# Kernel tuning notes

Measured on AMD Instinct MI355X. Metric: run time of the kernel, lower is better.

Reference implementation:

```python
import jax, jax.numpy as jnp
import numpy as np

ROPE_BASE = 1000.0  # note: module uses base=1000, not the usual 10000


def _rope(x):
    # x: [B, L, H, d]; rotates the full head dim (x_pass is empty since d == hid_head)
    d = x.shape[-1]
    L = x.shape[1]
    theta = 1.0 / (ROPE_BASE ** (jnp.arange(0, d, 2, dtype=jnp.float32) / d))  # [d/2]
    idx = jnp.arange(L, dtype=jnp.float32)[:, None] * theta[None, :]            # [L, d/2]
    idx2 = jnp.concatenate([idx, idx], axis=-1)                                 # [L, d]
    cos = jnp.cos(idx2)[:, None, :]  # [L, 1, d] -> broadcasts over B, H
    sin = jnp.sin(idx2)[:, None, :]
    half = d // 2
    neg_half = jnp.concatenate([-x[..., half:], x[..., :half]], axis=-1)
    return x * cos + neg_half * sin


def setup_inputs() -> dict:
    key = jax.random.key(0)
    ks = jax.random.split(key, 8)
    B, Lq, Lc, F = 4, 1024, 2047, 2048
    s = 0.02
    return {
        "kv": jax.random.normal(ks[0], (B, 1, F), jnp.float32),
        "q": jax.random.normal(ks[1], (B, Lq, F), jnp.float32),
        "kv_cache": jax.random.normal(ks[2], (B, Lc, F, 2), jnp.float32),
        "Wq": jax.random.normal(ks[3], (F, F), jnp.float32) * s,
        "Wk": jax.random.normal(ks[4], (F, F), jnp.float32) * s,
        "Wv": jax.random.normal(ks[5], (F, F), jnp.float32) * s,
        "Wo": jax.random.normal(ks[6], (F, F), jnp.float32) * s,
        "mask": jnp.ones((B, 1, Lq, Lc + 1), jnp.int32),
        "num_heads": 16,
    }


def reference(kv, q, kv_cache, Wq, Wk, Wv, Wo, mask, num_heads):
    B = q.shape[0]
    F = Wq.shape[1]
    hd = F // num_heads

    query = q @ Wq                          # [B, Lq, F]
    key_new = kv[:, -1, :] @ Wk             # [B, F] (only last kv token is projected)
    val_new = kv[:, -1, :] @ Wv             # [B, F]

    key = jnp.concatenate([kv_cache[..., 0], key_new[:, None, :]], axis=1)    # [B, Lk, F]
    value = jnp.concatenate([kv_cache[..., 1], val_new[:, None, :]], axis=1)  # [B, Lk, F]
    kv_cache_out = jnp.stack([key, value], axis=-1)                            # [B, Lk, F, 2]

    query = query.reshape(B, -1, num_heads, hd)   # [B, Lq, H, d]
    key = key.reshape(B, -1, num_heads, hd)       # [B, Lk, H, d]
    value = value.reshape(B, -1, num_heads, hd)   # [B, Lk, H, d]

    query = _rope(query)
    key = _rope(key)

    aw = jnp.einsum('bqhd,bkhd->bhqk', query, key) / jnp.sqrt(jnp.float32(hd))
    aw = jnp.where(mask > 0, aw, -jnp.inf)  # mask [B,1,Lq,Lk] broadcasts over heads
    aw = jax.nn.softmax(aw, axis=-1)

    out = jnp.einsum('bhqk,bkhd->bqhd', aw, value).reshape(B, -1, F)
    logits = out @ Wo
    return logits, kv_cache_out
```

## Files before the change

### kernel.cpp

```cpp
#include <hip/hip_runtime.h>

#define B_  4
#define LQ  1024
#define LC  2047
#define LK  2048
#define F_  2048
#define H_  16
#define DH  128
#define NT  (LK / 64)

typedef __attribute__((ext_vector_type(4))) float f32x4;
typedef __attribute__((ext_vector_type(8))) __bf16 bf16x8;
typedef __attribute__((ext_vector_type(8))) unsigned short u16x8;

#define GLD16(gp, lp)                                                          \
  __builtin_amdgcn_global_load_lds(                                            \
      (const __attribute__((address_space(1))) void*)(gp),                     \
      (__attribute__((address_space(3))) void*)(lp), 16, 0, 0)

__device__ __forceinline__ unsigned short f2bf(float f) {
  unsigned u = __float_as_uint(f);
  u += 0x7FFFu + ((u >> 16) & 1u);
  return (unsigned short)(u >> 16);
}
__device__ __forceinline__ float bf2f(unsigned short u) {
  return __uint_as_float((unsigned)u << 16);
}
__device__ __forceinline__ unsigned pack_bf2(float a, float b) {
  return (__float_as_uint(b) & 0xffff0000u) | (__float_as_uint(a) >> 16);
}

__global__ void k_tables(float* __restrict__ cost, float* __restrict__ sint) {
  int idx = blockIdx.x * 256 + threadIdx.x;
  int pos = idx >> 6, j = idx & 63;
  float theta = powf(1000.0f, -(float)j / 64.0f);
  float a = (float)pos * theta;
  cost[idx] = cosf(a);
  sint[idx] = sinf(a);
}

__global__ void k_gemv_part(const float* __restrict__ kv, const float* __restrict__ Wk,
                            const float* __restrict__ Wv, float* __restrict__ part) {
  __shared__ float kvs[4][256];
  int tid = threadIdx.x, z = blockIdx.z;
#pragma unroll
  for (int b = 0; b < 4; ++b) kvs[b][tid] = kv[b * F_ + z * 256 + tid];
  __syncthreads();
  const float* W = blockIdx.y ? Wv : Wk;
  int col = blockIdx.x * 256 + tid;
  float a0 = 0.f, a1 = 0.f, a2 = 0.f, a3 = 0.f;
  for (int k = 0; k < 256; ++k) {
    float w = W[(size_t)(z * 256 + k) * F_ + col];
    a0 = fmaf(kvs[0][k], w, a0);
    a1 = fmaf(kvs[1][k], w, a1);
    a2 = fmaf(kvs[2][k], w, a2);
    a3 = fmaf(kvs[3][k], w, a3);
  }
  float* o = part + (size_t)(blockIdx.y * 8 + z) * 8192;
  o[col] = a0; o[2048 + col] = a1; o[4096 + col] = a2; o[6144 + col] = a3;
}

__global__ void k_prep_kv(const float* __restrict__ cache, const float* __restrict__ gpart,
                          const float* __restrict__ cost, const float* __restrict__ sint,
                          float* __restrict__ cache_out,
                          unsigned short* __restrict__ Kr, unsigned short* __restrict__ Vb) {
  int t = blockIdx.x * 256 + threadIdx.x;
  int j = t & 63, h = (t >> 6) & 15, pos = (t >> 10) & 2047, b = t >> 21;
  int f = h * DH + j;
  float k1, v1, k2, v2;
  if (pos < LC) {
    const float* p = cache + ((size_t)(b * LC + pos) * F_ + f) * 2;
    float2 x = *(const float2*)p;
    float2 y = *(const float2*)(p + 128);
    k1 = x.x; v1 = x.y; k2 = y.x; v2 = y.y;
  } else {
    float s0 = 0.f, s1 = 0.f, s2 = 0.f, s3 = 0.f;
#pragma unroll
    for (int z = 0; z < 8; ++z) {
      const float* gk = gpart + (size_t)z * 8192 + b * 2048;
      const float* gv = gpart + (size_t)(8 + z) * 8192 + b * 2048;
      s0 += gk[f]; s1 += gk[f + 64];
      s2 += gv[f]; s3 += gv[f + 64];
    }
    k1 = s0; k2 = s1; v1 = s2; v2 = s3;
  }
  float* o = cache_out + ((size_t)(b * LK + pos) * F_ + f) * 2;
  *(float2*)o = make_float2(k1, v1);
  *(float2*)(o + 128) = make_float2(k2, v2);
  float c = cost[pos * 64 + j], s = sint[pos * 64 + j];
  size_t kb = ((size_t)(b * H_ + h) * LK + pos) * DH + j;
  Kr[kb]      = f2bf(k1 * c - k2 * s);
  Kr[kb + 64] = f2bf(k2 * c + k1 * s);
  Vb[kb]      = f2bf(v1);
  Vb[kb + 64] = f2bf(v2);
}

__global__ void k_transpose_w(const float* __restrict__ Wq, const float* __restrict__ Wo,
                              unsigned short* __restrict__ WqT, unsigned short* __restrict__ WoT) {
  __shared__ float tile[32][33];
  const float* W = blockIdx.z ? Wo : Wq;
  unsigned short* Wt = blockIdx.z ? WoT : WqT;
  int n0 = blockIdx.x * 32, k0 = blockIdx.y * 32;
  int tx = threadIdx.x & 31, ty = threadIdx.x >> 5;
#pragma unroll
  for (int p = 0; p < 4; ++p)
    tile[ty + p * 8][tx] = W[(size_t)(k0 + ty + p * 8) * F_ + n0 + tx];
  __syncthreads();
#pragma unroll
  for (int p = 0; p < 4; ++p)
    Wt[(size_t)(n0 + ty + p * 8) * F_ + k0 + tx] = f2bf(tile[tx][ty + p * 8]);
}

__global__ void k_q_bf16(const float* __restrict__ x, unsigned short* __restrict__ y) {
  int t = blockIdx.x * 256 + threadIdx.x;
  float4 v = ((const float4*)x)[t];
  ushort4 o;
  o.x = f2bf(v.x); o.y = f2bf(v.y); o.z = f2bf(v.z); o.w = f2bf(v.w);
  ((ushort4*)y)[t] = o;
}

template <int MODE>
__launch_bounds__(256)
__global__ void k_gemm(const unsigned short* __restrict__ A, const unsigned short* __restrict__ Bt,
                       void* __restrict__ Cv, const float* __restrict__ cost,
                       const float* __restrict__ sint, int M, int N, int K) {
  __shared__ __align__(16) unsigned short SMEM[16640];
  unsigned short* As = SMEM;
  unsigned short* Bs = SMEM + 4096;
  int tid = threadIdx.x, wid = tid >> 6, l = tid & 63;
  int wm = wid >> 1, wn = wid & 1;
  int lr = l & 15, lg = l >> 4;
  int m0 = blockIdx.y * 128, n0 = blockIdx.x * 128;
  int row0 = tid >> 2, ch = tid & 3;
  const unsigned short* ga0 = A  + (size_t)(m0 + row0) * K + ch * 8;
  const unsigned short* ga1 = A  + (size_t)(m0 + row0 + 64) * K + ch * 8;
  const unsigned short* gb0 = Bt + (size_t)(n0 + row0) * K + ch * 8;
  const unsigned short* gb1 = Bt + (size_t)(n0 + row0 + 64) * K + ch * 8;
  f32x4 acc[4][4];
#pragma unroll
  for (int i = 0; i < 4; ++i)
#pragma unroll
    for (int j = 0; j < 4; ++j) acc[i][j] = (f32x4){0.f, 0.f, 0.f, 0.f};

  for (int kt = 0; kt < K; kt += 32) {
    __syncthreads();
    GLD16(ga0 + kt, As + tid * 8);
    GLD16(ga1 + kt, As + (tid + 256) * 8);
    GLD16(gb0 + kt, Bs + tid * 8);
    GLD16(gb1 + kt, Bs + (tid + 256) * 8);
    __syncthreads();
    bf16x8 af[4], bfr[4];
#pragma unroll
    for (int i = 0; i < 4; ++i) {
      af[i]  = *(const bf16x8*)&As[(wm * 64 + i * 16 + lr) * 32 + lg * 8];
      bfr[i] = *(const bf16x8*)&Bs[(wn * 64 + i * 16 + lr) * 32 + lg * 8];
    }
    __builtin_amdgcn_s_setprio(1);
#pragma unroll
    for (int mi = 0; mi < 4; ++mi)
#pragma unroll
      for (int ni = 0; ni < 4; ++ni)
        acc[mi][ni] = __builtin_amdgcn_mfma_f32_16x16x32_bf16(af[mi], bfr[ni], acc[mi][ni], 0, 0, 0);
    __builtin_amdgcn_s_setprio(0);
  }

  if (MODE == 0) {
#pragma unroll
    for (int mi = 0; mi < 4; ++mi)
#pragma unroll
      for (int ni = 0; ni < 4; ++ni) {
        int row = m0 + wm * 64 + mi * 16 + lg * 4;
        int col = n0 + wn * 64 + ni * 16 + lr;
#pragma unroll
        for (int r = 0; r < 4; ++r)
          ((float*)Cv)[(size_t)(row + r) * N + col] = acc[mi][ni][r];
      }
  } else {
    unsigned short* X = SMEM;
    __syncthreads();
#pragma unroll
    for (int mi = 0; mi < 4; ++mi)
#pragma unroll
      for (int ni = 0; ni < 4; ++ni) {
        int lrow = wm * 64 + mi * 16 + lg * 4;
        int col = wn * 64 + ni * 16 + lr;
#pragma unroll
        for (int r = 0; r < 4; ++r)
          X[(lrow + r) * 130 + col] = f2bf(acc[mi][ni][r]);
      }
    __syncthreads();
    int h = blockIdx.x;
    const float scale = 0.12751743343788055f;
    unsigned short* Q = (unsigned short*)Cv;
#pragma unroll
    for (int mi = 0; mi < 4; ++mi) {
      int lrow0 = wm * 64 + mi * 16 + lg * 4;
#pragma unroll
      for (int r = 0; r < 4; ++r) {
        int lrow = lrow0 + r;
        int grow = m0 + lrow;
        int qi = grow & 1023, b = grow >> 10;
        size_t obase = ((size_t)(b * H_ + h) * LQ + qi) * DH;
#pragma unroll
        for (int ni = 0; ni < 4; ++ni) {
          int col = wn * 64 + ni * 16 + lr;
          int jj = col & 63;
          float c = cost[qi * 64 + jj], s = sint[qi * 64 + jj];
          float a = acc[mi][ni][r];
          float a2 = bf2f(X[lrow * 130 + (col ^ 64)]);
          float o = (col < 64) ? (a * c - a2 * s) : (a * c + a2 * s);
          Q[obase + col] = f2bf(o * scale);
        }
      }
    }
  }
}

__launch_bounds__(256, 2)
__global__ void k_attn(const unsigned short* __restrict__ Qr, const unsigned short* __restrict__ Kr,
                       const unsigned short* __restrict__ Vb, unsigned short* __restrict__ Oo) {
  __shared__ __align__(16) unsigned short KsB[2][64 * 128];
  __shared__ __align__(16) unsigned short Vt[128][72];
  __shared__ __align__(16) unsigned short Pb[4][32][72];
  int tid = threadIdx.x, wid = tid >> 6, l = tid & 63;
  int lr = l & 15, lg = l >> 4;
  int bh = blockIdx.x, q0 = blockIdx.y * 128 + wid * 32;
  const unsigned short* Qb = Qr + ((size_t)bh * LQ + q0) * DH;
  const unsigned short* Kb = Kr + (size_t)bh * LK * DH;
  const unsigned short* Vp = Vb + (size_t)bh * LK * DH;

  bf16x8 qf[2][4];
#pragma unroll
  for (int s = 0; s < 2; ++s)
#pragma unroll
    for (int c = 0; c < 4; ++c)
      qf[s][c] = *(const bf16x8*)(Qb + (size_t)(s * 16 + lr) * DH + c * 32 + lg * 8);

  int gkoff[4], lkoff[4];
#pragma unroll
  for (int p = 0; p < 4; ++p) {
    int g = tid + p * 256, row = g >> 4, cc = g & 15;
    gkoff[p] = row * DH + (cc ^ (row & 15)) * 8;
    lkoff[p] = g * 8;
  }

  f32x4 oacc[2][8];
#pragma unroll
  for (int s = 0; s < 2; ++s)
#pragma unroll
    for (int i = 0; i < 8; ++i) oacc[s][i] = (f32x4){0.f, 0.f, 0.f, 0.f};
  float mrun[2][4] = {{-1e30f, -1e30f, -1e30f, -1e30f}, {-1e30f, -1e30f, -1e30f, -1e30f}};
  float lpart[2][4] = {{0.f, 0.f, 0.f, 0.f}, {0.f, 0.f, 0.f, 0.f}};

  int kp = tid >> 4, cg = tid & 15;

#pragma unroll
  for (int p = 0; p < 4; ++p) GLD16(Kb + gkoff[p], &KsB[0][lkoff[p]]);
  const unsigned short* vs0 = Vp + (size_t)kp * DH + cg * 8;
  u16x8 v00 = *(const u16x8*)(vs0);
  u16x8 v01 = *(const u16x8*)(vs0 + 16 * DH);
  u16x8 v10 = *(const u16x8*)(vs0 + 32 * DH);
  u16x8 v11 = *(const u16x8*)(vs0 + 48 * DH);

  for (int kt = 0; kt < NT; ++kt) {
    int cur = kt & 1;
    asm volatile("s_waitcnt vmcnt(0)" ::: "memory");
    __builtin_amdgcn_sched_barrier(0);
    __builtin_amdgcn_s_barrier();
    __builtin_amdgcn_sched_barrier(0);

#pragma unroll
    for (int pp = 0; pp < 2; ++pp) {
      int j = kp + pp * 16;
      int kks = j ^ ((cg & 7) << 2);
      u16x8 a = pp ? v10 : v00, b2 = pp ? v11 : v01;
#pragma unroll
      for (int e = 0; e < 8; ++e) {
        unsigned pack = (unsigned)a[e] | ((unsigned)b2[e] << 16);
        *(unsigned*)&Vt[cg * 8 + e][kks * 2] = pack;
      }
    }
    {
      const unsigned short* Kn = Kb + (size_t)((kt + 1 < NT) ? (kt + 1) * 64 * DH : 0);
#pragma unroll
      for (int p = 0; p < 4; ++p) GLD16(Kn + gkoff[p], &KsB[cur ^ 1][lkoff[p]]);
    }
    {
      int tn = (kt + 1 < NT) ? kt + 1 : kt;
      const unsigned short* vn = Vp + (size_t)(tn * 64 + kp) * DH + cg * 8;
      v00 = *(const u16x8*)(vn);
      v01 = *(const u16x8*)(vn + 16 * DH);
      v10 = *(const u16x8*)(vn + 32 * DH);
      v11 = *(const u16x8*)(vn + 48 * DH);
    }
    asm volatile("s_waitcnt lgkmcnt(0)" ::: "memory");
    __builtin_amdgcn_sched_barrier(0);
    __builtin_amdgcn_s_barrier();
    __builtin_amdgcn_sched_barrier(0);

    const unsigned short* Kcur = KsB[cur];
    f32x4 sf[2][4];
    __builtin_amdgcn_s_setprio(1);
#pragma unroll
    for (int ct = 0; ct < 4; ++ct) {
      f32x4 s0 = (f32x4){0.f, 0.f, 0.f, 0.f};
      f32x4 s1 = (f32x4){0.f, 0.f, 0.f, 0.f};
#pragma unroll
      for (int ck = 0; ck < 4; ++ck) {
        bf16x8 kf = *(const bf16x8*)&Kcur[(ct * 16 + lr) * 128 + (((ck * 4 + lg) ^ lr) << 3)];
        s0 = __builtin_amdgcn_mfma_f32_16x16x32_bf16(qf[0][ck], kf, s0, 0, 0, 0);
        s1 = __builtin_amdgcn_mfma_f32_16x16x32_bf16(qf[1][ck], kf, s1, 0, 0, 0);
      }
      sf[0][ct] = s0; sf[1][ct] = s1;
    }
    __builtin_amdgcn_s_setprio(0);

    float pmax[2][4];
    bool allok = true;
#pragma unroll
    for (int s = 0; s < 2; ++s)
#pragma unroll
      for (int r = 0; r < 4; ++r) {
        pmax[s][r] = fmaxf(fmaxf(sf[s][0][r], sf[s][1][r]), fmaxf(sf[s][2][r], sf[s][3][r]));
        allok = allok && (pmax[s][r] - mrun[s][r] <= 8.0f);
      }
    if (!__all(allok)) {
#pragma unroll
      for (int s = 0; s < 2; ++s)
#pragma unroll
        for (int r = 0; r < 4; ++r) {
          float m = pmax[s][r];
#pragma unroll
          for (int off = 1; off < 16; off <<= 1) m = fmaxf(m, __shfl_xor(m, off));
          float mnew = fmaxf(mrun[s][r], m);
          float scl = exp2f(mrun[s][r] - mnew);
          lpart[s][r] *= scl;
#pragma unroll
          for (int dt = 0; dt < 8; ++dt) oacc[s][dt][r] *= scl;
          mrun[s][r] = mnew;
        }
    }
#pragma unroll
    for (int s = 0; s < 2; ++s)
#pragma unroll
      for (int r = 0; r < 4; ++r) {
        float p0 = exp2f(sf[s][0][r] - mrun[s][r]);
        float p1 = exp2f(sf[s][1][r] - mrun[s][r]);
        float p2 = exp2f(sf[s][2][r] - mrun[s][r]);
        float p3 = exp2f(sf[s][3][r] - mrun[s][r]);
        lpart[s][r] += (p0 + p1) + (p2 + p3);
        unsigned* row = (unsigned*)&Pb[wid][s * 16 + lg * 4 + r][0];
        row[lr]      = pack_bf2(p0, p1);
        row[16 + lr] = pack_bf2(p2, p3);
      }

    bf16x8 pf00 = *(const bf16x8*)&Pb[wid][lr][lg * 8];
    bf16x8 pf01 = *(const bf16x8*)&Pb[wid][lr][32 + lg * 8];
    bf16x8 pf10 = *(const bf16x8*)&Pb[wid][16 + lr][lg * 8];
    bf16x8 pf11 = *(const bf16x8*)&Pb[wid][16 + lr][32 + lg * 8];
    __builtin_amdgcn_s_setprio(1);
#pragma unroll
    for (int dt = 0; dt < 8; ++dt) {
      int d = dt * 16 + lr;
      int x = (d >> 3) & 7;
      bf16x8 v0 = *(const bf16x8*)&Vt[d][(lg ^ x) << 3];
      bf16x8 v1 = *(const bf16x8*)&Vt[d][((4 + lg) ^ x) << 3];
      oacc[0][dt] = __builtin_amdgcn_mfma_f32_16x16x32_bf16(pf00, v0, oacc[0][dt], 0, 0, 0);
      oacc[0][dt] = __builtin_amdgcn_mfma_f32_16x16x32_bf16(pf01, v1, oacc[0][dt], 0, 0, 0);
      oacc[1][dt] = __builtin_amdgcn_mfma_f32_16x16x32_bf16(pf10, v0, oacc[1][dt], 0, 0, 0);
      oacc[1][dt] = __builtin_amdgcn_mfma_f32_16x16x32_bf16(pf11, v1, oacc[1][dt], 0, 0, 0);
    }
    __builtin_amdgcn_s_setprio(0);
  }

  int b = bh >> 4, h = bh & 15;
#pragma unroll
  for (int s = 0; s < 2; ++s)
#pragma unroll
    for (int r = 0; r < 4; ++r) {
      float sum = lpart[s][r];
#pragma unroll
      for (int off = 1; off < 16; off <<= 1) sum += __shfl_xor(sum, off);
      float inv = 1.0f / sum;
      int qrow = q0 + s * 16 + lg * 4 + r;
      size_t base = ((size_t)(b * LQ + qrow)) * F_ + h * DH;
#pragma unroll
      for (int dt = 0; dt < 8; ++dt)
        Oo[base + dt * 16 + lr] = f2bf(oacc[s][dt][r] * inv);
    }
}

extern "C" void kernel_launch(void* const* d_in, const int* in_sizes, int n_in,
                              void* d_out, int out_size, void* d_ws, size_t ws_size,
                              hipStream_t stream) {
  const float* kv    = (const float*)d_in[0];
  const float* q     = (const float*)d_in[1];
  const float* cache = (const float*)d_in[2];
  const float* Wq    = (const float*)d_in[3];
  const float* Wk    = (const float*)d_in[4];
  const float* Wv    = (const float*)d_in[5];
  const float* Wo    = (const float*)d_in[6];

  float* logits    = (float*)d_out;
  float* cache_out = logits + (size_t)B_ * LQ * F_;

  char* ws = (char*)d_ws;
  float* cost          = (float*)(ws);
  float* sint          = (float*)(ws + 524288);
  float* gpart         = (float*)(ws + 1114112);
  unsigned short* WqT  = (unsigned short*)(ws + 1638400);
  unsigned short* WoT  = (unsigned short*)(ws + 10027008);
  unsigned short* qbf  = (unsigned short*)(ws + 18415616);
  unsigned short* Qro  = (unsigned short*)(ws + 35192832);
  unsigned short* Kro  = (unsigned short*)(ws + 51970048);
  unsigned short* Vbf  = (unsigned short*)(ws + 85524480);
  unsigned short* attno = (unsigned short*)(ws + 127467520);

  k_tables<<<dim3(512), dim3(256), 0, stream>>>(cost, sint);
  k_gemv_part<<<dim3(8, 2, 8), dim3(256), 0, stream>>>(kv, Wk, Wv, gpart);
  k_prep_kv<<<dim3(32768), dim3(256), 0, stream>>>(cache, gpart, cost, sint,
                                                   cache_out, Kro, Vbf);
  k_transpose_w<<<dim3(64, 64, 2), dim3(256), 0, stream>>>(Wq, Wo, WqT, WoT);
  k_q_bf16<<<dim3(8192), dim3(256), 0, stream>>>(q, qbf);
  k_gemm<2><<<dim3(16, 32), dim3(256), 0, stream>>>(qbf, WqT, Qro, cost, sint,
                                                    B_ * LQ, F_, F_);
  k_attn<<<dim3(64, 8), dim3(256), 0, stream>>>(Qro, Kro, Vbf, attno);
  k_gemm<0><<<dim3(16, 32), dim3(256), 0, stream>>>(attno, WoT, logits, nullptr, nullptr,
                                                    B_ * LQ, F_, F_);
}
```

Measured before the change: 317.8 us.

## Shrink attention q-tile to 16 rows per wave, single-buffer K for occupancy

Each wave in the attention kernel now handles 16 query rows instead of 32, so the block covers 64 rows and the grid doubles. K staging in LDS drops from double to single buffering, and the K load for the current tile is issued at the top of each iteration and waited on before the QK MFMAs. Launch bounds rise to 3 blocks per CU. The aim is to cut registers and LDS per block to raise occupancy and parallelism, at the cost of loading each K/V tile twice as often per query row and losing the K prefetch overlap.

```diff
diff --git a/kernel.cpp b/kernel.cpp
--- a/kernel.cpp
+++ b/kernel.cpp
@@ -216,25 +216,23 @@
   }
 }
 
-__launch_bounds__(256, 2)
+__launch_bounds__(256, 3)
 __global__ void k_attn(const unsigned short* __restrict__ Qr, const unsigned short* __restrict__ Kr,
                        const unsigned short* __restrict__ Vb, unsigned short* __restrict__ Oo) {
-  __shared__ __align__(16) unsigned short KsB[2][64 * 128];
+  __shared__ __align__(16) unsigned short Ks[64 * 128];
   __shared__ __align__(16) unsigned short Vt[128][72];
-  __shared__ __align__(16) unsigned short Pb[4][32][72];
+  __shared__ __align__(16) unsigned short Pb[4][16][72];
   int tid = threadIdx.x, wid = tid >> 6, l = tid & 63;
   int lr = l & 15, lg = l >> 4;
-  int bh = blockIdx.x, q0 = blockIdx.y * 128 + wid * 32;
+  int bh = blockIdx.x, q0 = blockIdx.y * 64 + wid * 16;
   const unsigned short* Qb = Qr + ((size_t)bh * LQ + q0) * DH;
   const unsigned short* Kb = Kr + (size_t)bh * LK * DH;
   const unsigned short* Vp = Vb + (size_t)bh * LK * DH;
 
-  bf16x8 qf[2][4];
-#pragma unroll
-  for (int s = 0; s < 2; ++s)
-#pragma unroll
-    for (int c = 0; c < 4; ++c)
-      qf[s][c] = *(const bf16x8*)(Qb + (size_t)(s * 16 + lr) * DH + c * 32 + lg * 8);
+  bf16x8 qf[4];
+#pragma unroll
+  for (int c = 0; c < 4; ++c)
+    qf[c] = *(const bf16x8*)(Qb + (size_t)lr * DH + c * 32 + lg * 8);
 
   int gkoff[4], lkoff[4];
 #pragma unroll
@@ -244,18 +242,14 @@
     lkoff[p] = g * 8;
   }
 
-  f32x4 oacc[2][8];
-#pragma unroll
-  for (int s = 0; s < 2; ++s)
-#pragma unroll
-    for (int i = 0; i < 8; ++i) oacc[s][i] = (f32x4){0.f, 0.f, 0.f, 0.f};
-  float mrun[2][4] = {{-1e30f, -1e30f, -1e30f, -1e30f}, {-1e30f, -1e30f, -1e30f, -1e30f}};
-  float lpart[2][4] = {{0.f, 0.f, 0.f, 0.f}, {0.f, 0.f, 0.f, 0.f}};
+  f32x4 oacc[8];
+#pragma unroll
+  for (int i = 0; i < 8; ++i) oacc[i] = (f32x4){0.f, 0.f, 0.f, 0.f};
+  float mrun[4] = {-1e30f, -1e30f, -1e30f, -1e30f};
+  float lpart[4] = {0.f, 0.f, 0.f, 0.f};
 
   int kp = tid >> 4, cg = tid & 15;
 
-#pragma unroll
-  for (int p = 0; p < 4; ++p) GLD16(Kb + gkoff[p], &KsB[0][lkoff[p]]);
   const unsigned short* vs0 = Vp + (size_t)kp * DH + cg * 8;
   u16x8 v00 = *(const u16x8*)(vs0);
   u16x8 v01 = *(const u16x8*)(vs0 + 16 * DH);
@@ -263,12 +257,13 @@
   u16x8 v11 = *(const u16x8*)(vs0 + 48 * DH);
 
   for (int kt = 0; kt < NT; ++kt) {
-    int cur = kt & 1;
-    asm volatile("s_waitcnt vmcnt(0)" ::: "memory");
-    __builtin_amdgcn_sched_barrier(0);
     __builtin_amdgcn_s_barrier();
     __builtin_amdgcn_sched_barrier(0);
-
+    {
+      const unsigned short* Kt = Kb + (size_t)kt * 64 * DH;
+#pragma unroll
+      for (int p = 0; p < 4; ++p) GLD16(Kt + gkoff[p], Ks + lkoff[p]);
+    }
 #pragma unroll
     for (int pp = 0; pp < 2; ++pp) {
       int j = kp + pp * 16;
@@ -279,11 +274,6 @@
         unsigned pack = (unsigned)a[e] | ((unsigned)b2[e] << 16);
         *(unsigned*)&Vt[cg * 8 + e][kks * 2] = pack;
       }
-    }
-    {
-      const unsigned short* Kn = Kb + (size_t)((kt + 1 < NT) ? (kt + 1) * 64 * DH : 0);
-#pragma unroll
-      for (int p = 0; p < 4; ++p) GLD16(Kn + gkoff[p], &KsB[cur ^ 1][lkoff[p]]);
     }
     {
       int tn = (kt + 1 < NT) ? kt + 1 : kt;
@@ -293,71 +283,60 @@
       v10 = *(const u16x8*)(vn + 32 * DH);
       v11 = *(const u16x8*)(vn + 48 * DH);
     }
-    asm volatile("s_waitcnt lgkmcnt(0)" ::: "memory");
+    asm volatile("s_waitcnt vmcnt(4) lgkmcnt(0)" ::: "memory");
     __builtin_amdgcn_sched_barrier(0);
     __builtin_amdgcn_s_barrier();
     __builtin_amdgcn_sched_barrier(0);
 
-    const unsigned short* Kcur = KsB[cur];
-    f32x4 sf[2][4];
+    f32x4 sf[4];
     __builtin_amdgcn_s_setprio(1);
 #pragma unroll
     for (int ct = 0; ct < 4; ++ct) {
       f32x4 s0 = (f32x4){0.f, 0.f, 0.f, 0.f};
-      f32x4 s1 = (f32x4){0.f, 0.f, 0.f, 0.f};
 #pragma unroll
       for (int ck = 0; ck < 4; ++ck) {
-        bf16x8 kf = *(const bf16x8*)&Kcur[(ct * 16 + lr) * 128 + (((ck * 4 + lg) ^ lr) << 3)];
-        s0 = __builtin_amdgcn_mfma_f32_16x16x32_bf16(qf[0][ck], kf, s0, 0, 0, 0);
-        s1 = __builtin_amdgcn_mfma_f32_16x16x32_bf16(qf[1][ck], kf, s1, 0, 0, 0);
-      }
-      sf[0][ct] = s0; sf[1][ct] = s1;
+        bf16x8 kf = *(const bf16x8*)&Ks[(ct * 16 + lr) * 128 + (((ck * 4 + lg) ^ lr) << 3)];
+        s0 = __builtin_amdgcn_mfma_f32_16x16x32_bf16(qf[ck], kf, s0, 0, 0, 0);
+      }
+      sf[ct] = s0;
     }
     __builtin_amdgcn_s_setprio(0);
 
-    float pmax[2][4];
+    float pmax[4];
     bool allok = true;
 #pragma unroll
-    for (int s = 0; s < 2; ++s)
+    for (int r = 0; r < 4; ++r) {
+      pmax[r] = fmaxf(fmaxf(sf[0][r], sf[1][r]), fmaxf(sf[2][r], sf[3][r]));
+      allok = allok && (pmax[r] - mrun[r] <= 8.0f);
+    }
+    if (!__all(allok)) {
 #pragma unroll
       for (int r = 0; r < 4; ++r) {
-        pmax[s][r] = fmaxf(fmaxf(sf[s][0][r], sf[s][1][r]), fmaxf(sf[s][2][r], sf[s][3][r]));
-        allok = allok && (pmax[s][r] - mrun[s][r] <= 8.0f);
-      }
-    if (!__all(allok)) {
-#pragma unroll
-      for (int s = 0; s < 2; ++s)
-#pragma unroll
-        for (int r = 0; r < 4; ++r) {
-          float m = pmax[s][r];
-#pragma unroll
-          for (int off = 1; off < 16; off <<= 1) m = fmaxf(m, __shfl_xor(m, off));
-          float mnew = fmaxf(mrun[s][r], m);
-          float scl = exp2f(mrun[s][r] - mnew);
-          lpart[s][r] *= scl;
-#pragma unroll
-          for (int dt = 0; dt < 8; ++dt) oacc[s][dt][r] *= scl;
-          mrun[s][r] = mnew;
-        }
-    }
-#pragma unroll
-    for (int s = 0; s < 2; ++s)
-#pragma unroll
-      for (int r = 0; r < 4; ++r) {
-        float p0 = exp2f(sf[s][0][r] - mrun[s][r]);
-        float p1 = exp2f(sf[s][1][r] - mrun[s][r]);
-        float p2 = exp2f(sf[s][2][r] - mrun[s][r]);
-        float p3 = exp2f(sf[s][3][r] - mrun[s][r]);
-        lpart[s][r] += (p0 + p1) + (p2 + p3);
-        unsigned* row = (unsigned*)&Pb[wid][s * 16 + lg * 4 + r][0];
-        row[lr]      = pack_bf2(p0, p1);
-        row[16 + lr] = pack_bf2(p2, p3);
-      }
-
-    bf16x8 pf00 = *(const bf16x8*)&Pb[wid][lr][lg * 8];
-    bf16x8 pf01 = *(const bf16x8*)&Pb[wid][lr][32 + lg * 8];
-    bf16x8 pf10 = *(const bf16x8*)&Pb[wid][16 + lr][lg * 8];
-    bf16x8 pf11 = *(const bf16x8*)&Pb[wid][16 + lr][32 + lg * 8];
+        float m = pmax[r];
+#pragma unroll
+        for (int off = 1; off < 16; off <<= 1) m = fmaxf(m, __shfl_xor(m, off));
+        float mnew = fmaxf(mrun[r], m);
+        float scl = exp2f(mrun[r] - mnew);
+        lpart[r] *= scl;
+#pragma unroll
+        for (int dt = 0; dt < 8; ++dt) oacc[dt][r] *= scl;
+        mrun[r] = mnew;
+      }
+    }
+#pragma unroll
+    for (int r = 0; r < 4; ++r) {
+      float p0 = exp2f(sf[0][r] - mrun[r]);
+      float p1 = exp2f(sf[1][r] - mrun[r]);
+      float p2 = exp2f(sf[2][r] - mrun[r]);
+      float p3 = exp2f(sf[3][r] - mrun[r]);
+      lpart[r] += (p0 + p1) + (p2 + p3);
+      unsigned* row = (unsigned*)&Pb[wid][lg * 4 + r][0];
+      row[lr]      = pack_bf2(p0, p1);
+      row[16 + lr] = pack_bf2(p2, p3);
+    }
+
+    bf16x8 pf0 = *(const bf16x8*)&Pb[wid][lr][lg * 8];
+    bf16x8 pf1 = *(const bf16x8*)&Pb[wid][lr][32 + lg * 8];
     __builtin_amdgcn_s_setprio(1);
 #pragma unroll
     for (int dt = 0; dt < 8; ++dt) {
@@ -365,29 +344,25 @@
       int x = (d >> 3) & 7;
       bf16x8 v0 = *(const bf16x8*)&Vt[d][(lg ^ x) << 3];
       bf16x8 v1 = *(const bf16x8*)&Vt[d][((4 + lg) ^ x) << 3];
-      oacc[0][dt] = __builtin_amdgcn_mfma_f32_16x16x32_bf16(pf00, v0, oacc[0][dt], 0, 0, 0);
-      oacc[0][dt] = __builtin_amdgcn_mfma_f32_16x16x32_bf16(pf01, v1, oacc[0][dt], 0, 0, 0);
-      oacc[1][dt] = __builtin_amdgcn_mfma_f32_16x16x32_bf16(pf10, v0, oacc[1][dt], 0, 0, 0);
-      oacc[1][dt] = __builtin_amdgcn_mfma_f32_16x16x32_bf16(pf11, v1, oacc[1][dt], 0, 0, 0);
+      oacc[dt] = __builtin_amdgcn_mfma_f32_16x16x32_bf16(pf0, v0, oacc[dt], 0, 0, 0);
+      oacc[dt] = __builtin_amdgcn_mfma_f32_16x16x32_bf16(pf1, v1, oacc[dt], 0, 0, 0);
     }
     __builtin_amdgcn_s_setprio(0);
   }
 
   int b = bh >> 4, h = bh & 15;
 #pragma unroll
-  for (int s = 0; s < 2; ++s)
-#pragma unroll
-    for (int r = 0; r < 4; ++r) {
-      float sum = lpart[s][r];
-#pragma unroll
-      for (int off = 1; off < 16; off <<= 1) sum += __shfl_xor(sum, off);
-      float inv = 1.0f / sum;
-      int qrow = q0 + s * 16 + lg * 4 + r;
-      size_t base = ((size_t)(b * LQ + qrow)) * F_ + h * DH;
-#pragma unroll
-      for (int dt = 0; dt < 8; ++dt)
-        Oo[base + dt * 16 + lr] = f2bf(oacc[s][dt][r] * inv);
-    }
+  for (int r = 0; r < 4; ++r) {
+    float sum = lpart[r];
+#pragma unroll
+    for (int off = 1; off < 16; off <<= 1) sum += __shfl_xor(sum, off);
+    float inv = 1.0f / sum;
+    int qrow = q0 + lg * 4 + r;
+    size_t base = ((size_t)(b * LQ + qrow)) * F_ + h * DH;
+#pragma unroll
+    for (int dt = 0; dt < 8; ++dt)
+      Oo[base + dt * 16 + lr] = f2bf(oacc[dt][r] * inv);
+  }
 }
 
 extern "C" void kernel_launch(void* const* d_in, const int* in_sizes, int n_in,
@@ -424,7 +399,7 @@
   k_q_bf16<<<dim3(8192), dim3(256), 0, stream>>>(q, qbf);
   k_gemm<2><<<dim3(16, 32), dim3(256), 0, stream>>>(qbf, WqT, Qro, cost, sint,
                                                     B_ * LQ, F_, F_);
-  k_attn<<<dim3(64, 8), dim3(256), 0, stream>>>(Qro, Kro, Vbf, attno);
+  k_attn<<<dim3(64, 16), dim3(256), 0, stream>>>(Qro, Kro, Vbf, attno);
   k_gemm<0><<<dim3(16, 32), dim3(256), 0, stream>>>(attno, WoT, logits, nullptr, nullptr,
                                                     B_ * LQ, F_, F_);
 }
```

Result: slower. 352.8 us (+11.0%).
